# Kernel optimization log

Hardware: AMD Instinct MI355X
Metric: run time of the kernel (lower is better)

Reference implementation:

```python
import jax, jax.numpy as jnp
import numpy as np

N = 50000   # nodes
E = 1600000 # edges
K = 5       # Chebyshev order
F_IN, H1, H2, P = 32, 32, 16, 12


def setup_inputs() -> dict:
    key = jax.random.key(0)
    ks = jax.random.split(key, 16)
    x = jax.random.normal(ks[0], (N, F_IN), dtype=jnp.float32)
    edge_index = jax.random.randint(ks[1], (2, E), 0, N, dtype=jnp.int64)
    edge_weight = jax.random.uniform(ks[2], (E,), dtype=jnp.float32)
    s = 0.1
    # Cell 1: 3 gates (z, r, h), each with x-conv [K,F_IN,H1] and h-conv [K,H1,H1]
    Wx1 = jax.random.normal(ks[3], (3, K, F_IN, H1), dtype=jnp.float32) * s
    bx1 = jax.random.normal(ks[4], (3, H1), dtype=jnp.float32) * s
    Wh1 = jax.random.normal(ks[5], (3, K, H1, H1), dtype=jnp.float32) * s
    bh1 = jax.random.normal(ks[6], (3, H1), dtype=jnp.float32) * s
    # Cell 2
    Wx2 = jax.random.normal(ks[7], (3, K, H1, H2), dtype=jnp.float32) * s
    bx2 = jax.random.normal(ks[8], (3, H2), dtype=jnp.float32) * s
    Wh2 = jax.random.normal(ks[9], (3, K, H2, H2), dtype=jnp.float32) * s
    bh2 = jax.random.normal(ks[10], (3, H2), dtype=jnp.float32) * s
    # Output linear (torch convention: weight [out,in])
    Wl = jax.random.normal(ks[11], (P, H2), dtype=jnp.float32) * s
    bl = jax.random.normal(ks[12], (P,), dtype=jnp.float32) * s
    return dict(x=x, edge_index=edge_index, edge_weight=edge_weight,
                Wx1=Wx1, bx1=bx1, Wh1=Wh1, bh1=bh1,
                Wx2=Wx2, bx2=bx2, Wh2=Wh2, bh2=bh2, Wl=Wl, bl=bl)


def _cheb_norm(edge_index, edge_weight):
    # ChebConv 'sym' norm with lambda_max=2: L_hat off-diagonal = -D^-1/2 A D^-1/2,
    # diagonal cancels to 0 (get_laplacian +1 self loop, add_self_loops fill -1).
    row, col = edge_index[0], edge_index[1]
    deg = jax.ops.segment_sum(edge_weight, row, num_segments=N)
    dis = jnp.where(deg > 0, jax.lax.rsqrt(jnp.maximum(deg, 1e-30)), 0.0)
    return -dis[row] * edge_weight * dis[col]


def _gconv_gru_forward(x, edge_index, edge_weight, Wx1, bx1, Wh1, bh1,
                       Wx2, bx2, Wh2, bh2, Wl, bl):
    row, col = edge_index[0], edge_index[1]
    wn = _cheb_norm(edge_index, edge_weight)

    def spmm(v):  # (L_hat @ v): gather source rows, scatter-add to targets
        return jax.ops.segment_sum(v[row] * wn[:, None], col, num_segments=N)

    def cheb(v, W, b):  # W: [K, Fin, Fout]
        Tx0 = v
        out = Tx0 @ W[0]
        Tx1 = spmm(Tx0)
        out = out + Tx1 @ W[1]
        for k in range(2, K):
            Tx2 = 2.0 * spmm(Tx1) - Tx0
            out = out + Tx2 @ W[k]
            Tx0, Tx1 = Tx1, Tx2
        return out + b

    def gru_cell(v, H, Wx, bx, Wh, bh):
        Z = jax.nn.sigmoid(cheb(v, Wx[0], bx[0]) + cheb(H, Wh[0], bh[0]))
        R = jax.nn.sigmoid(cheb(v, Wx[1], bx[1]) + cheb(H, Wh[1], bh[1]))
        Ht = jnp.tanh(cheb(v, Wx[2], bx[2]) + cheb(H * R, Wh[2], bh[2]))
        return Z * H + (1.0 - Z) * Ht

    h = gru_cell(x, jnp.zeros((N, H1), x.dtype), Wx1, bx1, Wh1, bh1)
    h = jax.nn.relu(h)  # dropout is identity in eval mode
    h = gru_cell(h, jnp.zeros((N, H2), x.dtype), Wx2, bx2, Wh2, bh2)
    h = jax.nn.relu(h)
    return h @ Wl.T + bl


def reference(x, edge_index, edge_weight, Wx1, bx1, Wh1, bh1,
              Wx2, bx2, Wh2, bh2, Wl, bl):
    return _gconv_gru_forward(x, edge_index, edge_weight, Wx1, bx1, Wh1, bh1,
                              Wx2, bx2, Wh2, bh2, Wl, bl)
```

## Files before the change

### kernel.cpp

```cpp
#include <hip/hip_runtime.h>
#include <math.h>

#define NN 50000
#define NE 1600000
#define KORD 5
#define NB 196
#define QTR 12500
#define GE 782
#define MT 64
#define NBK 1563
#define NBP 1600
#define NCH 256
#define ECH (NE / NCH)
#define EC4 (NE / 64)
#define PADE 1800192

#define SCALE_W 2097152.0f
#define INV_SCALE_W (1.0f / 2097152.0f)
#define SCALE_D 4194304.0f
#define INV_SCALE_D (1.0f / 4194304.0f)

typedef _Float16 half8 __attribute__((ext_vector_type(8)));
typedef _Float16 half4v __attribute__((ext_vector_type(4)));
typedef float float4v __attribute__((ext_vector_type(4)));

__global__ __launch_bounds__(1024) void k_deg(const int* __restrict__ ei,
                                              const float* __restrict__ ew,
                                              int* __restrict__ deg_g) {
    __shared__ int h[QTR];
    int q = blockIdx.x >> 6, ch = blockIdx.x & 63;
    for (int i = threadIdx.x; i < QTR; i += 1024) h[i] = 0;
    __syncthreads();
    int base = ch * EC4, lo = q * QTR;
    for (int e = base + threadIdx.x; e < base + EC4; e += 1024) {
        int li = ei[e] - lo;
        if ((unsigned)li < (unsigned)QTR)
            atomicAdd(&h[li], __float2int_rn(ew[e] * SCALE_D));
    }
    __syncthreads();
    int* outp = deg_g + blockIdx.x * QTR;
    for (int i = threadIdx.x; i < QTR; i += 1024) outp[i] = h[i];
}

__global__ __launch_bounds__(256) void k_dis2(const int* __restrict__ deg_g,
                                              float* __restrict__ dis) {
    int n = blockIdx.x * 256 + threadIdx.x;
    if (n >= NN) return;
    int q = n / QTR, i = n % QTR;
    const int* p = deg_g + (q * 64) * QTR + i;
    int s = 0;
#pragma unroll
    for (int c = 0; c < 64; c++) s += p[c * QTR];
    float d = (float)s * INV_SCALE_D;
    dis[n] = s > 0 ? rsqrtf(fmaxf(d, 1e-30f)) : 0.f;
}

__global__ __launch_bounds__(256) void k_cvt(const float* __restrict__ x,
                                             _Float16* __restrict__ x16) {
    int i = blockIdx.x * 256 + threadIdx.x;
    if (i < NN * 8) {
        float4 v = ((const float4*)x)[i];
        half4v h = {(_Float16)v.x, (_Float16)v.y, (_Float16)v.z, (_Float16)v.w};
        *(half4v*)(x16 + i * 4) = h;
    }
}

__global__ __launch_bounds__(1024) void k_bhist(const int* __restrict__ ei,
                                                int* __restrict__ bh) {
    __shared__ int hist[NBK];
    int ch = blockIdx.x;
    for (int i = threadIdx.x; i < NBK; i += 1024) hist[i] = 0;
    __syncthreads();
    const int* cols = ei + NE;
    int base = ch * ECH;
    for (int e = base + threadIdx.x; e < base + ECH; e += 1024)
        atomicAdd(&hist[cols[e] >> 5], 1);
    __syncthreads();
    int* outp = bh + ch * NBP;
    for (int b = threadIdx.x; b < NBK; b += 1024) outp[b] = hist[b];
}

__global__ __launch_bounds__(256) void k_btot(const int* __restrict__ bh,
                                              int* __restrict__ tot) {
    int b = blockIdx.x * 256 + threadIdx.x;
    if (b >= NBP) return;
    int s = 0;
    if (b < NBK) {
#pragma unroll 8
        for (int ch = 0; ch < NCH; ch++) s += bh[ch * NBP + b];
    }
    tot[b] = s;
}

__global__ __launch_bounds__(1024) void k_bscan1(const int* __restrict__ tot,
                                                 int* __restrict__ off_bk) {
    __shared__ int s[1024];
    int t = threadIdx.x;
    int a0 = (2 * t < NBP) ? tot[2 * t] : 0;
    int a1 = (2 * t + 1 < NBP) ? tot[2 * t + 1] : 0;
    int p0 = (a0 + 127) & ~127;
    int p1 = (a1 + 127) & ~127;
    s[t] = p0 + p1;
    __syncthreads();
    for (int d = 1; d < 1024; d <<= 1) {
        int u = (t >= d) ? s[t - d] : 0;
        __syncthreads();
        s[t] += u;
        __syncthreads();
    }
    int excl = (t == 0) ? 0 : s[t - 1];
    if (2 * t < NBK) off_bk[2 * t] = excl;
    if (2 * t + 1 < NBK) off_bk[2 * t + 1] = excl + p0;
    if (t == 1023) off_bk[NBK] = s[1023];
}

__global__ __launch_bounds__(256) void k_bcur(int* __restrict__ bh,
                                              const int* __restrict__ off_bk) {
    int b = blockIdx.x * 256 + threadIdx.x;
    if (b >= NBK) return;
    int run = off_bk[b];
    for (int ch = 0; ch < NCH; ch++) {
        int v = bh[ch * NBP + b];
        bh[ch * NBP + b] = run;
        run += v;
    }
}

__global__ __launch_bounds__(128) void k_pad(const int* __restrict__ off_bk,
                                             const int* __restrict__ tot,
                                             int2* __restrict__ edges) {
    int b = blockIdx.x;
    int start = off_bk[b] + tot[b];
    int end = off_bk[b + 1];
    for (int i = start + threadIdx.x; i < end; i += 128)
        edges[i] = make_int2(0, 0);
}

__global__ __launch_bounds__(1024) void k_cperm(const int* __restrict__ ei,
                                                const float* __restrict__ ew,
                                                const float* __restrict__ dis,
                                                const int* __restrict__ bh,
                                                int2* __restrict__ edges) {
    __shared__ int cur[NBK];
    int ch = blockIdx.x;
    const int* cp = bh + ch * NBP;
    for (int b = threadIdx.x; b < NBK; b += 1024) cur[b] = cp[b];
    __syncthreads();
    int base = ch * ECH;
    for (int e = base + threadIdx.x; e < base + ECH; e += 1024) {
        int r = ei[e], c = ei[NE + e];
        float w = -dis[r] * ew[e] * dis[c];
        int pos = atomicAdd(&cur[c >> 5], 1);
        int packed = (int)((unsigned)r | ((unsigned)(c & 31) << 16));
        edges[pos] = make_int2(packed, __float_as_int(w));
    }
}

#define SPMM_DS(C0, W0, G0, C1, W1, G1, C2, W2, G2, C3, W3, G3)      \
    {                                                                 \
        int* a0 = &acc[C0][sub * 4];                                  \
        int* a1 = &acc[C1][sub * 4];                                  \
        int* a2 = &acc[C2][sub * 4];                                  \
        int* a3 = &acc[C3][sub * 4];                                  \
        atomicAdd(a0 + 0, __float2int_rn(W0 * (float)G0.x));          \
        atomicAdd(a0 + 1, __float2int_rn(W0 * (float)G0.y));          \
        atomicAdd(a0 + 2, __float2int_rn(W0 * (float)G0.z));          \
        atomicAdd(a0 + 3, __float2int_rn(W0 * (float)G0.w));          \
        atomicAdd(a1 + 0, __float2int_rn(W1 * (float)G1.x));          \
        atomicAdd(a1 + 1, __float2int_rn(W1 * (float)G1.y));          \
        atomicAdd(a1 + 2, __float2int_rn(W1 * (float)G1.z));          \
        atomicAdd(a1 + 3, __float2int_rn(W1 * (float)G1.w));          \
        atomicAdd(a2 + 0, __float2int_rn(W2 * (float)G2.x));          \
        atomicAdd(a2 + 1, __float2int_rn(W2 * (float)G2.y));          \
        atomicAdd(a2 + 2, __float2int_rn(W2 * (float)G2.z));          \
        atomicAdd(a2 + 3, __float2int_rn(W2 * (float)G2.w));          \
        atomicAdd(a3 + 0, __float2int_rn(W3 * (float)G3.x));          \
        atomicAdd(a3 + 1, __float2int_rn(W3 * (float)G3.y));          \
        atomicAdd(a3 + 2, __float2int_rn(W3 * (float)G3.z));          \
        atomicAdd(a3 + 3, __float2int_rn(W3 * (float)G3.w));          \
    }

struct h4 { half4v v; };

__global__ __launch_bounds__(256) void k_spmm(const int* __restrict__ off_bk,
                                              const int2* __restrict__ edges,
                                              const _Float16* __restrict__ vin16,
                                              const float* __restrict__ prev,
                                              float* __restrict__ vout,
                                              _Float16* __restrict__ vout16,
                                              float scale) {
    __shared__ int acc[32][33];
    int b = blockIdx.x;
    for (int i = threadIdx.x; i < 32 * 33; i += 256) (&acc[0][0])[i] = 0;
    __syncthreads();
    int e0 = off_bk[b], e1 = off_bk[b + 1];
    int group = threadIdx.x >> 3, sub = threadIdx.x & 7;
    const h4* vin4 = (const h4*)vin16;
    int i = e0 + group;
    if (i < e1) {
        int2 R0 = edges[i], R1 = edges[i + 32], R2 = edges[i + 64], R3 = edges[i + 96];
        half4v G0, G1, G2, G3;
        int C0 = 0, C1 = 0, C2 = 0, C3 = 0;
        float W0 = 0.f, W1 = 0.f, W2 = 0.f, W3 = 0.f;
        bool haveG = false;
        while (true) {
            int ni = i + 128;
            bool moreR = ni < e1;
            int2 N0, N1, N2, N3;
            if (moreR) {
                N0 = edges[ni]; N1 = edges[ni + 32];
                N2 = edges[ni + 64]; N3 = edges[ni + 96];
            }
            half4v g0 = vin4[((unsigned)R0.x & 0xffffu) * 8 + sub].v;
            half4v g1 = vin4[((unsigned)R1.x & 0xffffu) * 8 + sub].v;
            half4v g2 = vin4[((unsigned)R2.x & 0xffffu) * 8 + sub].v;
            half4v g3 = vin4[((unsigned)R3.x & 0xffffu) * 8 + sub].v;
            if (haveG) SPMM_DS(C0, W0, G0, C1, W1, G1, C2, W2, G2, C3, W3, G3);
            C0 = (unsigned)R0.x >> 16; C1 = (unsigned)R1.x >> 16;
            C2 = (unsigned)R2.x >> 16; C3 = (unsigned)R3.x >> 16;
            W0 = __int_as_float(R0.y) * SCALE_W;
            W1 = __int_as_float(R1.y) * SCALE_W;
            W2 = __int_as_float(R2.y) * SCALE_W;
            W3 = __int_as_float(R3.y) * SCALE_W;
            G0 = g0; G1 = g1; G2 = g2; G3 = g3;
            haveG = true;
            if (!moreR) break;
            R0 = N0; R1 = N1; R2 = N2; R3 = N3;
            i = ni;
        }
        SPMM_DS(C0, W0, G0, C1, W1, G1, C2, W2, G2, C3, W3, G3);
    }
    __syncthreads();
    float sf = scale * INV_SCALE_W;
    int base = b << 5;
    int nl = threadIdx.x >> 3, s4 = threadIdx.x & 7;
    int n = base + nl;
    if (n < NN) {
        const int* a = &acc[nl][s4 * 4];
        float4 o;
        if (prev) {
            float4 p = ((const float4*)prev)[n * 8 + s4];
            o = make_float4(fmaf(sf, (float)a[0], -p.x),
                            fmaf(sf, (float)a[1], -p.y),
                            fmaf(sf, (float)a[2], -p.z),
                            fmaf(sf, (float)a[3], -p.w));
        } else {
            o = make_float4(sf * (float)a[0], sf * (float)a[1],
                            sf * (float)a[2], sf * (float)a[3]);
        }
        if (vout) ((float4*)vout)[n * 8 + s4] = o;
        half4v oh = {(_Float16)o.x, (_Float16)o.y, (_Float16)o.z, (_Float16)o.w};
        *(half4v*)(vout16 + n * 32 + s4 * 4) = oh;
    }
}

__global__ __launch_bounds__(256) void k_epi1(
    const _Float16* __restrict__ x16, const _Float16* __restrict__ t1,
    const _Float16* __restrict__ t2, const _Float16* __restrict__ t3,
    const _Float16* __restrict__ t4, const float* __restrict__ Wx1,
    const float* __restrict__ bx1, const float* __restrict__ bh1,
    float* __restrict__ h, _Float16* __restrict__ h16) {
    __shared__ _Float16 T[5][MT][40];
    __shared__ _Float16 Wt[64][168];
    int n0 = blockIdx.x * MT;
    const _Float16* bufs[5] = {x16, t1, t2, t3, t4};
#pragma unroll
    for (int b = 0; b < 5; b++) {
        for (int idx = threadIdx.x; idx < MT * 4; idx += 256) {
            int r = idx >> 2, c8 = idx & 3;
            int rr = n0 + r; if (rr >= NN) rr = NN - 1;
            half8 v = *(const half8*)(bufs[b] + rr * 32 + c8 * 8);
            *(half8*)&T[b][r][c8 * 8] = v;
        }
    }
    const float* Wz = Wx1;
    const float* Wh = Wx1 + 2 * KORD * 32 * 32;
    for (int idx = threadIdx.x; idx < 160 * 64; idx += 256) {
        int k = idx >> 6, n = idx & 63;
        int b = k >> 5, i = k & 31;
        float w = (n < 32) ? Wz[b * 1024 + i * 32 + n]
                           : Wh[b * 1024 + i * 32 + (n - 32)];
        Wt[n][k] = (_Float16)w;
    }
    __syncthreads();
    int wave = threadIdx.x >> 6;
    int lane = threadIdx.x & 63;
    int lo = lane & 15, quad = lane >> 4;
    float4v acc[4];
#pragma unroll
    for (int t = 0; t < 4; t++) acc[t] = (float4v){0.f, 0.f, 0.f, 0.f};
#pragma unroll
    for (int b = 0; b < 5; b++) {
        half8 a = *(half8*)&T[b][wave * 16 + lo][quad * 8];
#pragma unroll
        for (int t = 0; t < 4; t++) {
            half8 bf = *(half8*)&Wt[t * 16 + lo][b * 32 + quad * 8];
            acc[t] = __builtin_amdgcn_mfma_f32_16x16x32_f16(a, bf, acc[t], 0, 0, 0);
        }
    }
    int nd_base = n0 + wave * 16 + quad * 4;
#pragma unroll
    for (int t = 0; t < 2; t++) {
        int j = t * 16 + lo;
        float bz = bx1[j] + bh1[j];
        float bhb = bx1[64 + j] + bh1[64 + j];
#pragma unroll
        for (int reg = 0; reg < 4; reg++) {
            int nd = nd_base + reg;
            if (nd < NN) {
                float zz = acc[t][reg] + bz;
                float hh = acc[t + 2][reg] + bhb;
                float z = 1.f / (1.f + __expf(-zz));
                float tt = __expf(-2.f * fabsf(hh));
                float ht = copysignf((1.f - tt) / (1.f + tt), hh);
                float v = fmaxf((1.f - z) * ht, 0.f);
                h[nd * 32 + j] = v;
                h16[nd * 32 + j] = (_Float16)v;
            }
        }
    }
}

__global__ __launch_bounds__(256) void k_epi2(
    const _Float16* __restrict__ h16, const _Float16* __restrict__ t1,
    const _Float16* __restrict__ t2, const _Float16* __restrict__ t3,
    const _Float16* __restrict__ t4, const float* __restrict__ Wx2,
    const float* __restrict__ bx2, const float* __restrict__ bh2,
    const float* __restrict__ Wl, const float* __restrict__ bl,
    float* __restrict__ out) {
    __shared__ _Float16 T[5][MT][40];
    __shared__ _Float16 Wt[32][168];
    __shared__ float H2[MT][17];
    int n0 = blockIdx.x * MT;
    const _Float16* bufs[5] = {h16, t1, t2, t3, t4};
#pragma unroll
    for (int b = 0; b < 5; b++) {
        for (int idx = threadIdx.x; idx < MT * 4; idx += 256) {
            int r = idx >> 2, c8 = idx & 3;
            int rr = n0 + r; if (rr >= NN) rr = NN - 1;
            half8 v = *(const half8*)(bufs[b] + rr * 32 + c8 * 8);
            *(half8*)&T[b][r][c8 * 8] = v;
        }
    }
    const float* Wz = Wx2;
    const float* Wh = Wx2 + 2 * KORD * 32 * 16;
    for (int idx = threadIdx.x; idx < 160 * 32; idx += 256) {
        int k = idx >> 5, n = idx & 31;
        int b = k >> 5, i = k & 31;
        float w = (n < 16) ? Wz[b * 512 + i * 16 + n]
                           : Wh[b * 512 + i * 16 + (n - 16)];
        Wt[n][k] = (_Float16)w;
    }
    __syncthreads();
    int wave = threadIdx.x >> 6;
    int lane = threadIdx.x & 63;
    int lo = lane & 15, quad = lane >> 4;
    float4v acc[2];
    acc[0] = (float4v){0.f, 0.f, 0.f, 0.f};
    acc[1] = (float4v){0.f, 0.f, 0.f, 0.f};
#pragma unroll
    for (int b = 0; b < 5; b++) {
        half8 a = *(half8*)&T[b][wave * 16 + lo][quad * 8];
#pragma unroll
        for (int t = 0; t < 2; t++) {
            half8 bf = *(half8*)&Wt[t * 16 + lo][b * 32 + quad * 8];
            acc[t] = __builtin_amdgcn_mfma_f32_16x16x32_f16(a, bf, acc[t], 0, 0, 0);
        }
    }
    {
        int j = lo;
        float bz = bx2[j] + bh2[j];
        float bhb = bx2[32 + j] + bh2[32 + j];
        int ndl_base = wave * 16 + quad * 4;
#pragma unroll
        for (int reg = 0; reg < 4; reg++) {
            float zz = acc[0][reg] + bz;
            float hh = acc[1][reg] + bhb;
            float z = 1.f / (1.f + __expf(-zz));
            float tt = __expf(-2.f * fabsf(hh));
            float ht = copysignf((1.f - tt) / (1.f + tt), hh);
            H2[ndl_base + reg][j] = fmaxf((1.f - z) * ht, 0.f);
        }
    }
    __syncthreads();
    for (int idx = threadIdx.x; idx < MT * 12; idx += 256) {
        int n = idx / 12, p = idx % 12;
        int gn = n0 + n;
        if (gn < NN) {
            float o = bl[p];
#pragma unroll
            for (int jj = 0; jj < 16; jj++) o = fmaf(H2[n][jj], Wl[p * 16 + jj], o);
            out[gn * 12 + p] = o;
        }
    }
}


extern "C" void kernel_launch(void* const* d_in, const int* in_sizes, int n_in,
                              void* d_out, int out_size, void* d_ws, size_t ws_size,
                              hipStream_t stream) {
    const float* x   = (const float*)d_in[0];
    const int*   ei  = (const int*)d_in[1];
    const float* ew  = (const float*)d_in[2];
    const float* Wx1 = (const float*)d_in[3];
    const float* bx1 = (const float*)d_in[4];
    const float* bh1 = (const float*)d_in[6];
    const float* Wx2 = (const float*)d_in[7];
    const float* bx2 = (const float*)d_in[8];
    const float* bh2 = (const float*)d_in[10];
    const float* Wl  = (const float*)d_in[11];
    const float* bl  = (const float*)d_in[12];
    float* out = (float*)d_out;

    float* ws     = (float*)d_ws;
    float* dis    = ws;
    int*   bh     = (int*)(ws + 50048);
    int*   tot    = bh + NCH * NBP;
    int*   off_bk = tot + NBP;
    int2*  edges  = (int2*)(off_bk + NBP);
    float* T1     = (float*)(edges + PADE);
    float* T2     = T1 + NN * 32;
    float* T3     = T2 + NN * 32;
    float* hb     = T3 + NN * 32;
    _Float16* x16 = (_Float16*)(hb + NN * 32);
    _Float16* t1h = x16 + NN * 32;
    _Float16* t2h = t1h + NN * 32;
    _Float16* t3h = t2h + NN * 32;
    _Float16* t4h = t3h + NN * 32;
    _Float16* hbh = t4h + NN * 32;
    int*   deg_g  = (int*)T1;

    k_deg  <<<256, 1024, 0, stream>>>(ei, ew, deg_g);
    k_dis2 <<<NB, 256, 0, stream>>>(deg_g, dis);
    k_cvt  <<<(NN * 8 + 255) / 256, 256, 0, stream>>>(x, x16);
    k_bhist<<<NCH, 1024, 0, stream>>>(ei, bh);
    k_btot <<<7, 256, 0, stream>>>(bh, tot);
    k_bscan1<<<1, 1024, 0, stream>>>(tot, off_bk);
    k_bcur <<<7, 256, 0, stream>>>(bh, off_bk);
    k_pad  <<<NBK, 128, 0, stream>>>(off_bk, tot, edges);
    k_cperm<<<NCH, 1024, 0, stream>>>(ei, ew, dis, bh, edges);

    k_spmm<<<NBK, 256, 0, stream>>>(off_bk, edges, x16, nullptr, T1, t1h, 1.f);
    k_spmm<<<NBK, 256, 0, stream>>>(off_bk, edges, t1h, x,      T2, t2h, 2.f);
    k_spmm<<<NBK, 256, 0, stream>>>(off_bk, edges, t2h, T1,     T3, t3h, 2.f);
    k_spmm<<<NBK, 256, 0, stream>>>(off_bk, edges, t3h, T2, nullptr, t4h, 2.f);
    k_epi1<<<GE, 256, 0, stream>>>(x16, t1h, t2h, t3h, t4h, Wx1, bx1, bh1, hb, hbh);

    k_spmm<<<NBK, 256, 0, stream>>>(off_bk, edges, hbh, nullptr, T1, t1h, 1.f);
    k_spmm<<<NBK, 256, 0, stream>>>(off_bk, edges, t1h, hb,     T2, t2h, 2.f);
    k_spmm<<<NBK, 256, 0, stream>>>(off_bk, edges, t2h, T1,     T3, t3h, 2.f);
    k_spmm<<<NBK, 256, 0, stream>>>(off_bk, edges, t3h, T2, nullptr, t4h, 2.f);
    k_epi2<<<GE, 256, 0, stream>>>(hbh, t1h, t2h, t3h, t4h, Wx2, bx2, bh2, Wl, bl, out);
}
```

Baseline: 345.9 us.

## Drop fp32 Chebyshev buffers, widen SpMM gathers to half8, fold padding into bcur

The fp32 copies of the Chebyshev terms and of the hidden state are removed. The recurrence's previous term is now read from the fp16 buffers, which cuts global writes and reads in every SpMM pass. The SpMM gather now uses 4 threads per edge with 16-byte half8 loads, two edges in flight per group instead of four. The separate padding kernel is folded into k_bcur, which zeroes the pad serially per thread, saving one launch. The cost is fp16 rounding on the subtracted previous term, which may compound over the recurrence, plus fewer independent loads in flight per thread.

Result: no change. 351.7 us (+1.7%).

```diff
diff --git a/kernel.cpp b/kernel.cpp
--- a/kernel.cpp
+++ b/kernel.cpp
@@ -115,7 +115,8 @@
 }
 
 __global__ __launch_bounds__(256) void k_bcur(int* __restrict__ bh,
-                                              const int* __restrict__ off_bk) {
+                                              const int* __restrict__ off_bk,
+                                              int2* __restrict__ edges) {
     int b = blockIdx.x * 256 + threadIdx.x;
     if (b >= NBK) return;
     int run = off_bk[b];
@@ -124,16 +125,8 @@
         bh[ch * NBP + b] = run;
         run += v;
     }
-}
-
-__global__ __launch_bounds__(128) void k_pad(const int* __restrict__ off_bk,
-                                             const int* __restrict__ tot,
-                                             int2* __restrict__ edges) {
-    int b = blockIdx.x;
-    int start = off_bk[b] + tot[b];
     int end = off_bk[b + 1];
-    for (int i = start + threadIdx.x; i < end; i += 128)
-        edges[i] = make_int2(0, 0);
+    for (int i = run; i < end; i++) edges[i] = make_int2(0, 0);
 }
 
 __global__ __launch_bounds__(1024) void k_cperm(const int* __restrict__ ei,
@@ -156,37 +149,23 @@
     }
 }
 
-#define SPMM_DS(C0, W0, G0, C1, W1, G1, C2, W2, G2, C3, W3, G3)      \
+#define SPMM_DS1(C, W, G)                                             \
     {                                                                 \
-        int* a0 = &acc[C0][sub * 4];                                  \
-        int* a1 = &acc[C1][sub * 4];                                  \
-        int* a2 = &acc[C2][sub * 4];                                  \
-        int* a3 = &acc[C3][sub * 4];                                  \
-        atomicAdd(a0 + 0, __float2int_rn(W0 * (float)G0.x));          \
-        atomicAdd(a0 + 1, __float2int_rn(W0 * (float)G0.y));          \
-        atomicAdd(a0 + 2, __float2int_rn(W0 * (float)G0.z));          \
-        atomicAdd(a0 + 3, __float2int_rn(W0 * (float)G0.w));          \
-        atomicAdd(a1 + 0, __float2int_rn(W1 * (float)G1.x));          \
-        atomicAdd(a1 + 1, __float2int_rn(W1 * (float)G1.y));          \
-        atomicAdd(a1 + 2, __float2int_rn(W1 * (float)G1.z));          \
-        atomicAdd(a1 + 3, __float2int_rn(W1 * (float)G1.w));          \
-        atomicAdd(a2 + 0, __float2int_rn(W2 * (float)G2.x));          \
-        atomicAdd(a2 + 1, __float2int_rn(W2 * (float)G2.y));          \
-        atomicAdd(a2 + 2, __float2int_rn(W2 * (float)G2.z));          \
-        atomicAdd(a2 + 3, __float2int_rn(W2 * (float)G2.w));          \
-        atomicAdd(a3 + 0, __float2int_rn(W3 * (float)G3.x));          \
-        atomicAdd(a3 + 1, __float2int_rn(W3 * (float)G3.y));          \
-        atomicAdd(a3 + 2, __float2int_rn(W3 * (float)G3.z));          \
-        atomicAdd(a3 + 3, __float2int_rn(W3 * (float)G3.w));          \
-    }
-
-struct h4 { half4v v; };
+        int* a = &acc[C][sub * 8];                                    \
+        atomicAdd(a + 0, __float2int_rn(W * (float)G[0]));            \
+        atomicAdd(a + 1, __float2int_rn(W * (float)G[1]));            \
+        atomicAdd(a + 2, __float2int_rn(W * (float)G[2]));            \
+        atomicAdd(a + 3, __float2int_rn(W * (float)G[3]));            \
+        atomicAdd(a + 4, __float2int_rn(W * (float)G[4]));            \
+        atomicAdd(a + 5, __float2int_rn(W * (float)G[5]));            \
+        atomicAdd(a + 6, __float2int_rn(W * (float)G[6]));            \
+        atomicAdd(a + 7, __float2int_rn(W * (float)G[7]));            \
+    }
 
 __global__ __launch_bounds__(256) void k_spmm(const int* __restrict__ off_bk,
                                               const int2* __restrict__ edges,
                                               const _Float16* __restrict__ vin16,
-                                              const float* __restrict__ prev,
-                                              float* __restrict__ vout,
+                                              const _Float16* __restrict__ prev16,
                                               _Float16* __restrict__ vout16,
                                               float scale) {
     __shared__ int acc[32][33];
@@ -194,41 +173,33 @@
     for (int i = threadIdx.x; i < 32 * 33; i += 256) (&acc[0][0])[i] = 0;
     __syncthreads();
     int e0 = off_bk[b], e1 = off_bk[b + 1];
-    int group = threadIdx.x >> 3, sub = threadIdx.x & 7;
-    const h4* vin4 = (const h4*)vin16;
+    int group = threadIdx.x >> 2, sub = threadIdx.x & 3;
+    const half8* vin8 = (const half8*)vin16;
     int i = e0 + group;
     if (i < e1) {
-        int2 R0 = edges[i], R1 = edges[i + 32], R2 = edges[i + 64], R3 = edges[i + 96];
-        half4v G0, G1, G2, G3;
-        int C0 = 0, C1 = 0, C2 = 0, C3 = 0;
-        float W0 = 0.f, W1 = 0.f, W2 = 0.f, W3 = 0.f;
+        int2 R0 = edges[i], R1 = edges[i + 64];
+        half8 G0, G1;
+        int C0 = 0, C1 = 0;
+        float W0 = 0.f, W1 = 0.f;
         bool haveG = false;
         while (true) {
             int ni = i + 128;
             bool moreR = ni < e1;
-            int2 N0, N1, N2, N3;
-            if (moreR) {
-                N0 = edges[ni]; N1 = edges[ni + 32];
-                N2 = edges[ni + 64]; N3 = edges[ni + 96];
-            }
-            half4v g0 = vin4[((unsigned)R0.x & 0xffffu) * 8 + sub].v;
-            half4v g1 = vin4[((unsigned)R1.x & 0xffffu) * 8 + sub].v;
-            half4v g2 = vin4[((unsigned)R2.x & 0xffffu) * 8 + sub].v;
-            half4v g3 = vin4[((unsigned)R3.x & 0xffffu) * 8 + sub].v;
-            if (haveG) SPMM_DS(C0, W0, G0, C1, W1, G1, C2, W2, G2, C3, W3, G3);
+            int2 N0, N1;
+            if (moreR) { N0 = edges[ni]; N1 = edges[ni + 64]; }
+            half8 g0 = vin8[((unsigned)R0.x & 0xffffu) * 4 + sub];
+            half8 g1 = vin8[((unsigned)R1.x & 0xffffu) * 4 + sub];
+            if (haveG) { SPMM_DS1(C0, W0, G0); SPMM_DS1(C1, W1, G1); }
             C0 = (unsigned)R0.x >> 16; C1 = (unsigned)R1.x >> 16;
-            C2 = (unsigned)R2.x >> 16; C3 = (unsigned)R3.x >> 16;
             W0 = __int_as_float(R0.y) * SCALE_W;
             W1 = __int_as_float(R1.y) * SCALE_W;
-            W2 = __int_as_float(R2.y) * SCALE_W;
-            W3 = __int_as_float(R3.y) * SCALE_W;
-            G0 = g0; G1 = g1; G2 = g2; G3 = g3;
+            G0 = g0; G1 = g1;
             haveG = true;
             if (!moreR) break;
-            R0 = N0; R1 = N1; R2 = N2; R3 = N3;
+            R0 = N0; R1 = N1;
             i = ni;
         }
-        SPMM_DS(C0, W0, G0, C1, W1, G1, C2, W2, G2, C3, W3, G3);
+        SPMM_DS1(C0, W0, G0); SPMM_DS1(C1, W1, G1);
     }
     __syncthreads();
     float sf = scale * INV_SCALE_W;
@@ -237,19 +208,18 @@
     int n = base + nl;
     if (n < NN) {
         const int* a = &acc[nl][s4 * 4];
-        float4 o;
-        if (prev) {
-            float4 p = ((const float4*)prev)[n * 8 + s4];
-            o = make_float4(fmaf(sf, (float)a[0], -p.x),
-                            fmaf(sf, (float)a[1], -p.y),
-                            fmaf(sf, (float)a[2], -p.z),
-                            fmaf(sf, (float)a[3], -p.w));
+        float ox, oy, oz, ow;
+        if (prev16) {
+            half4v p = *(const half4v*)(prev16 + n * 32 + s4 * 4);
+            ox = fmaf(sf, (float)a[0], -(float)p[0]);
+            oy = fmaf(sf, (float)a[1], -(float)p[1]);
+            oz = fmaf(sf, (float)a[2], -(float)p[2]);
+            ow = fmaf(sf, (float)a[3], -(float)p[3]);
         } else {
-            o = make_float4(sf * (float)a[0], sf * (float)a[1],
-                            sf * (float)a[2], sf * (float)a[3]);
-        }
-        if (vout) ((float4*)vout)[n * 8 + s4] = o;
-        half4v oh = {(_Float16)o.x, (_Float16)o.y, (_Float16)o.z, (_Float16)o.w};
+            ox = sf * (float)a[0]; oy = sf * (float)a[1];
+            oz = sf * (float)a[2]; ow = sf * (float)a[3];
+        }
+        half4v oh = {(_Float16)ox, (_Float16)oy, (_Float16)oz, (_Float16)ow};
         *(half4v*)(vout16 + n * 32 + s4 * 4) = oh;
     }
 }
@@ -259,7 +229,7 @@
     const _Float16* __restrict__ t2, const _Float16* __restrict__ t3,
     const _Float16* __restrict__ t4, const float* __restrict__ Wx1,
     const float* __restrict__ bx1, const float* __restrict__ bh1,
-    float* __restrict__ h, _Float16* __restrict__ h16) {
+    _Float16* __restrict__ h16) {
     __shared__ _Float16 T[5][MT][40];
     __shared__ _Float16 Wt[64][168];
     int n0 = blockIdx.x * MT;
@@ -313,9 +283,7 @@
                 float z = 1.f / (1.f + __expf(-zz));
                 float tt = __expf(-2.f * fabsf(hh));
                 float ht = copysignf((1.f - tt) / (1.f + tt), hh);
-                float v = fmaxf((1.f - z) * ht, 0.f);
-                h[nd * 32 + j] = v;
-                h16[nd * 32 + j] = (_Float16)v;
+                h16[nd * 32 + j] = (_Float16)fmaxf((1.f - z) * ht, 0.f);
             }
         }
     }
@@ -418,17 +386,13 @@
     int*   tot    = bh + NCH * NBP;
     int*   off_bk = tot + NBP;
     int2*  edges  = (int2*)(off_bk + NBP);
-    float* T1     = (float*)(edges + PADE);
-    float* T2     = T1 + NN * 32;
-    float* T3     = T2 + NN * 32;
-    float* hb     = T3 + NN * 32;
-    _Float16* x16 = (_Float16*)(hb + NN * 32);
+    _Float16* x16 = (_Float16*)(edges + PADE);
     _Float16* t1h = x16 + NN * 32;
     _Float16* t2h = t1h + NN * 32;
     _Float16* t3h = t2h + NN * 32;
     _Float16* t4h = t3h + NN * 32;
     _Float16* hbh = t4h + NN * 32;
-    int*   deg_g  = (int*)T1;
+    int*   deg_g  = (int*)x16;
 
     k_deg  <<<256, 1024, 0, stream>>>(ei, ew, deg_g);
     k_dis2 <<<NB, 256, 0, stream>>>(deg_g, dis);
@@ -436,19 +400,18 @@
     k_bhist<<<NCH, 1024, 0, stream>>>(ei, bh);
     k_btot <<<7, 256, 0, stream>>>(bh, tot);
     k_bscan1<<<1, 1024, 0, stream>>>(tot, off_bk);
-    k_bcur <<<7, 256, 0, stream>>>(bh, off_bk);
-    k_pad  <<<NBK, 128, 0, stream>>>(off_bk, tot, edges);
+    k_bcur <<<7, 256, 0, stream>>>(bh, off_bk, edges);
     k_cperm<<<NCH, 1024, 0, stream>>>(ei, ew, dis, bh, edges);
 
-    k_spmm<<<NBK, 256, 0, stream>>>(off_bk, edges, x16, nullptr, T1, t1h, 1.f);
-    k_spmm<<<NBK, 256, 0, stream>>>(off_bk, edges, t1h, x,      T2, t2h, 2.f);
-    k_spmm<<<NBK, 256, 0, stream>>>(off_bk, edges, t2h, T1,     T3, t3h, 2.f);
-    k_spmm<<<NBK, 256, 0, stream>>>(off_bk, edges, t3h, T2, nullptr, t4h, 2.f);
-    k_epi1<<<GE, 256, 0, stream>>>(x16, t1h, t2h, t3h, t4h, Wx1, bx1, bh1, hb, hbh);
-
-    k_spmm<<<NBK, 256, 0, stream>>>(off_bk, edges, hbh, nullptr, T1, t1h, 1.f);
-    k_spmm<<<NBK, 256, 0, stream>>>(off_bk, edges, t1h, hb,     T2, t2h, 2.f);
-    k_spmm<<<NBK, 256, 0, stream>>>(off_bk, edges, t2h, T1,     T3, t3h, 2.f);
-    k_spmm<<<NBK, 256, 0, stream>>>(off_bk, edges, t3h, T2, nullptr, t4h, 2.f);
+    k_spmm<<<NBK, 256, 0, stream>>>(off_bk, edges, x16, nullptr, t1h, 1.f);
+    k_spmm<<<NBK, 256, 0, stream>>>(off_bk, edges, t1h, x16,     t2h, 2.f);
+    k_spmm<<<NBK, 256, 0, stream>>>(off_bk, edges, t2h, t1h,     t3h, 2.f);
+    k_spmm<<<NBK, 256, 0, stream>>>(off_bk, edges, t3h, t2h,     t4h, 2.f);
+    k_epi1<<<GE, 256, 0, stream>>>(x16, t1h, t2h, t3h, t4h, Wx1, bx1, bh1, hbh);
+
+    k_spmm<<<NBK, 256, 0, stream>>>(off_bk, edges, hbh, nullptr, t1h, 1.f);
+    k_spmm<<<NBK, 256, 0, stream>>>(off_bk, edges, t1h, hbh,     t2h, 2.f);
+    k_spmm<<<NBK, 256, 0, stream>>>(off_bk, edges, t2h, t1h,     t3h, 2.f);
+    k_spmm<<<NBK, 256, 0, stream>>>(off_bk, edges, t3h, t2h,     t4h, 2.f);
     k_epi2<<<GE, 256, 0, stream>>>(hbh, t1h, t2h, t3h, t4h, Wx2, bx2, bh2, Wl, bl, out);
 }
```
